# Performance work log

Hardware: AMD Instinct MI355X
Metric: run time of the kernel (lower is better)

## Reference

```python
import jax, jax.numpy as jnp
import numpy as np

N_TREES, DEPTH, INPUT_DIM, N_CLASSES = 15, 3, 128, 10
N_LEAVES = 2 ** DEPTH
N_INTERNAL = N_LEAVES - 1


def _path_masks(depth):
    """Right/left ancestor indicator matrices [n_leaves, n_internal]."""
    n_leaves = 2 ** depth
    n_int = n_leaves - 1
    R = np.zeros((n_leaves, n_int), np.float32)
    L = np.zeros((n_leaves, n_int), np.float32)
    for leaf in range(n_leaves):
        node = leaf + n_int
        for _ in range(depth):
            parent = (node - 1) // 2
            if node % 2 == 0:
                R[leaf, parent] = 1.0
            else:
                L[leaf, parent] = 1.0
            node = parent
    return R, L

_R, _L = _path_masks(DEPTH)


def setup_inputs() -> dict:
    key = jax.random.key(0)
    k1, k2 = jax.random.split(key)
    batch = 262144
    per_tree = N_INTERNAL * INPUT_DIM + N_INTERNAL + N_LEAVES * N_CLASSES
    total = N_TREES * per_tree + N_TREES
    x = jax.random.normal(k1, (batch, INPUT_DIM), dtype=jnp.float32)
    params = jax.random.normal(k2, (total,), dtype=jnp.float32)
    return {"x": x, "params": params}


def reference(x, params):
    per_tree = N_INTERNAL * INPUT_DIM + N_INTERNAL + N_LEAVES * N_CLASSES
    blocks = params[: N_TREES * per_tree].reshape(N_TREES, per_tree)
    w_end = N_INTERNAL * INPUT_DIM
    split_w = blocks[:, :w_end].reshape(N_TREES, N_INTERNAL, INPUT_DIM)
    split_b = blocks[:, w_end : w_end + N_INTERNAL]  # [T, n_internal]
    leaf_logits = blocks[:, w_end + N_INTERNAL :].reshape(N_TREES, N_LEAVES, N_CLASSES)
    tree_w_logits = params[N_TREES * per_tree :]  # [T]

    # split logits z: [B, T, n_internal]
    z = jnp.einsum("bd,tnd->btn", x, split_w) + split_b[None, :, :]
    log_p = jax.nn.log_sigmoid(z)        # log sigma(z)
    log_1mp = jax.nn.log_sigmoid(-z)     # log (1 - sigma(z))

    R = jnp.asarray(_R)
    L = jnp.asarray(_L)
    # path product in log domain: [B, T, n_leaves]
    leaf_probs = jnp.exp(
        jnp.einsum("btn,ln->btl", log_p, R) + jnp.einsum("btn,ln->btl", log_1mp, L)
    )

    leaf_class_probs = jax.nn.softmax(leaf_logits, axis=-1)  # [T, n_leaves, C]
    tree_pred = jnp.einsum("btl,tlc->btc", leaf_probs, leaf_class_probs)
    tree_weights = jax.nn.softmax(tree_w_logits, axis=0)     # [T]
    final_pred = jnp.einsum("btc,t->bc", tree_pred, tree_weights)
    return final_pred
```

## Files before the change

### kernel.cpp

```cpp
#include <hip/hip_runtime.h>
#include <hip/hip_fp16.h>


typedef float    f32x4 __attribute__((ext_vector_type(4)));
typedef _Float16 half8 __attribute__((ext_vector_type(8)));

#define TREES      15
#define IDIM       128
#define NCLS       10
#define NINT       7
#define NLVS       8
#define PER_TREE   (NINT*IDIM + NINT + NLVS*NCLS)
#define NODES      (TREES*NINT)
#define NPAD       112
#define KPAD       128
#define RSTR       272
#define WSTR       4352
#define NBLK       512

__global__ __launch_bounds__(256) void prep_kernel(const float* __restrict__ p,
                                                   _Float16* __restrict__ wq,
                                                   float* __restrict__ bq,
                                                   _Float16* __restrict__ wbT) {
    const int gid  = blockIdx.x * 256 + threadIdx.x;
    const int nthr = gridDim.x * 256;

    for (int i = gid; i < NPAD * IDIM; i += nthr) {
        int g = i >> 7, k = i & 127;
        float v = 0.f;
        if (g < NODES) {
            int t = g / NINT, n = g % NINT;
            v = p[t * PER_TREE + n * IDIM + k];
        }
        wq[i] = (_Float16)v;
    }
    for (int i = gid; i < NPAD; i += nthr) {
        float v = 0.f;
        if (i < NODES) {
            int t = i / NINT, n = i % NINT;
            v = p[t * PER_TREE + NINT * IDIM + n];
        }
        bq[i] = v;
    }
    const float* tl = p + TREES * PER_TREE;
    for (int i = gid; i < 16 * KPAD; i += nthr) {
        int c = i >> 7, k = i & 127;
        float v = 0.f;
        if (c < NCLS && k < TREES * NLVS) {
            int t = k >> 3, l = k & 7;
            const float* ll = p + t * PER_TREE + NINT * IDIM + NINT + l * NCLS;
            float mx = ll[0];
            #pragma unroll
            for (int j = 1; j < NCLS; ++j) mx = fmaxf(mx, ll[j]);
            float se = 0.f;
            #pragma unroll
            for (int j = 0; j < NCLS; ++j) se += __expf(ll[j] - mx);
            float lsm = __expf(ll[c] - mx) / se;

            float m2 = tl[0];
            #pragma unroll
            for (int j = 1; j < TREES; ++j) m2 = fmaxf(m2, tl[j]);
            float s2 = 0.f;
            #pragma unroll
            for (int j = 0; j < TREES; ++j) s2 += __expf(tl[j] - m2);
            float tw = __expf(tl[t] - m2) / s2;
            v = lsm * tw;
        }
        wbT[i] = (_Float16)v;
    }
}

__device__ __forceinline__ void load_xa(const float* __restrict__ xr,
                                        f32x4 (&xa)[8]) {
    #pragma unroll
    for (int s = 0; s < 4; ++s) {
        xa[2 * s]     = *(const f32x4*)(xr + 32 * s);
        xa[2 * s + 1] = *(const f32x4*)(xr + 32 * s + 4);
    }
}

__global__ __launch_bounds__(256, 2) void tree_main(const float* __restrict__ x,
                                                    const _Float16* __restrict__ wq,
                                                    const float* __restrict__ bq,
                                                    const _Float16* __restrict__ wbT,
                                                    float* __restrict__ out,
                                                    int tpb) {
    __shared__ __align__(16) char lds[4 * WSTR];

    const int tid  = threadIdx.x;
    const int lane = tid & 63;
    const int w    = tid >> 6;
    const int lm   = lane & 15;
    const int lq   = lane >> 4;
    const int rg   = lane >> 2;
    const int g    = lane & 3;

    char* sbuf = &lds[w * WSTR];
    const long tile0 = (long)blockIdx.x * tpb;

    const float* xlane = x + (tile0 * 64 + 16 * w + lm) * IDIM + 8 * lq;

    f32x4 xaA[8], xaB[8];
    load_xa(xlane, xaA);

    half8 bf[7][4];
    float bb[7];
    #pragma unroll
    for (int nt = 0; nt < 7; ++nt) {
        bb[nt] = bq[16 * nt + lm];
        #pragma unroll
        for (int s = 0; s < 4; ++s)
            bf[nt][s] = *reinterpret_cast<const half8*>(wq + (16 * nt + lm) * IDIM + 32 * s + 8 * lq);
    }
    half8 wbf[4];
    #pragma unroll
    for (int s = 0; s < 4; ++s)
        wbf[s] = *reinterpret_cast<const half8*>(wbT + lm * KPAD + 32 * s + 8 * lq);

    auto tile_body = [&](int i, f32x4 (&xac)[8], f32x4 (&xan)[8]) {
        const long grow = (tile0 + i) * 64;

        half8 af[4];
        #pragma unroll
        for (int s = 0; s < 4; ++s) {
            half8 a;
            #pragma unroll
            for (int j = 0; j < 4; ++j) {
                a[j]     = (_Float16)xac[2 * s][j];
                a[j + 4] = (_Float16)xac[2 * s + 1][j];
            }
            af[s] = a;
        }

        if (i + 1 < tpb)
            load_xa(xlane + (long)(i + 1) * 64 * IDIM, xan);

        #pragma unroll
        for (int nt = 0; nt < 7; ++nt) {
            f32x4 acc = {bb[nt], bb[nt], bb[nt], bb[nt]};
            #pragma unroll
            for (int s = 0; s < 4; ++s)
                acc = __builtin_amdgcn_mfma_f32_16x16x32_f16(af[s], bf[nt][s], acc, 0, 0, 0);
            int node = 16 * nt + lm;
            int col  = node + ((node * 9363) >> 16);
            #pragma unroll
            for (int r = 0; r < 4; ++r) {
                float z  = acc[r];
                float sg = __builtin_amdgcn_rcpf(1.0f + __expf(-z));
                *(_Float16*)(sbuf + (4 * lq + r) * RSTR + col * 2) = (_Float16)sg;
            }
        }

        {
            const char* rowp = sbuf + rg * RSTR;
            half8 hv[4];
            #pragma unroll
            for (int tt = 0; tt < 4; ++tt)
                hv[tt] = *(const half8*)(rowp + 64 * g + 16 * tt);
            half8 lv[4];
            #pragma unroll
            for (int tt = 0; tt < 4; ++tt) {
                float s0 = (float)hv[tt][0], s1 = (float)hv[tt][1], s2v = (float)hv[tt][2];
                float s3 = (float)hv[tt][3], s4 = (float)hv[tt][4], s5 = (float)hv[tt][5];
                float s6 = (float)hv[tt][6];
                float u1 = 1.f - s0, u2 = s0;
                float q1 = u1 * s1, q0 = u1 - q1;
                float q3 = u2 * s2v, q2 = u2 - q3;
                float L1 = q0 * s3, L0 = q0 - L1;
                float L3 = q1 * s4, L2 = q1 - L3;
                float L5 = q2 * s5, L4 = q2 - L5;
                float L7 = q3 * s6, L6 = q3 - L7;
                float m = (4 * g + tt < TREES) ? 1.f : 0.f;
                half8 lv8;
                lv8[0] = (_Float16)(L0 * m); lv8[1] = (_Float16)(L1 * m);
                lv8[2] = (_Float16)(L2 * m); lv8[3] = (_Float16)(L3 * m);
                lv8[4] = (_Float16)(L4 * m); lv8[5] = (_Float16)(L5 * m);
                lv8[6] = (_Float16)(L6 * m); lv8[7] = (_Float16)(L7 * m);
                lv[tt] = lv8;
            }
            #pragma unroll
            for (int tt = 0; tt < 4; ++tt)
                *(half8*)(sbuf + rg * RSTR + 64 * g + 16 * tt) = lv[tt];
        }

        {
            half8 af2[4];
            #pragma unroll
            for (int s = 0; s < 4; ++s)
                af2[s] = *(const half8*)(sbuf + lm * RSTR + 64 * s + 16 * lq);
            f32x4 a2 = {0.f, 0.f, 0.f, 0.f};
            #pragma unroll
            for (int s = 0; s < 4; ++s)
                a2 = __builtin_amdgcn_mfma_f32_16x16x32_f16(af2[s], wbf[s], a2, 0, 0, 0);
            if (lm < NCLS) {
                #pragma unroll
                for (int r = 0; r < 4; ++r)
                    out[(grow + 16 * w + 4 * lq + r) * NCLS + lm] = a2[r];
            }
        }
    };

    for (int i = 0; i < tpb; i += 2) {
        tile_body(i,     xaA, xaB);
        tile_body(i + 1, xaB, xaA);
    }
}

extern "C" void kernel_launch(void* const* d_in, const int* in_sizes, int n_in,
                              void* d_out, int out_size, void* d_ws, size_t ws_size,
                              hipStream_t stream) {
    const float* x      = (const float*)d_in[0];
    const float* params = (const float*)d_in[1];
    float* out = (float*)d_out;

    _Float16* wq  = (_Float16*)d_ws;
    float*    bq  = (float*)((char*)d_ws + NPAD * IDIM * 2);
    _Float16* wbT = (_Float16*)((char*)bq + NPAD * 4);

    const int batch = in_sizes[0] / IDIM;
    const int tiles = batch / 64;
    const int tpb   = tiles / NBLK;

    prep_kernel<<<8, 256, 0, stream>>>(params, wq, bq, wbT);
    tree_main<<<NBLK, 256, 0, stream>>>(x, wq, bq, wbT, out, tpb);
}
```

Measured before the change: 208.4 us.

## Stage split weights in swizzled LDS and double block size for occupancy

```diff
diff --git a/kernel.cpp b/kernel.cpp
--- a/kernel.cpp
+++ b/kernel.cpp
@@ -79,13 +79,14 @@
     }
 }
 
-__global__ __launch_bounds__(256, 2) void tree_main(const float* __restrict__ x,
+__global__ __launch_bounds__(512, 4) void tree_main(const float* __restrict__ x,
                                                     const _Float16* __restrict__ wq,
                                                     const float* __restrict__ bq,
                                                     const _Float16* __restrict__ wbT,
                                                     float* __restrict__ out,
                                                     int tpb) {
-    __shared__ __align__(16) char lds[4 * WSTR];
+    __shared__ __align__(16) char lwq[NPAD * 256];
+    __shared__ __align__(16) char sls[8 * WSTR];
 
     const int tid  = threadIdx.x;
     const int lane = tid & 63;
@@ -95,30 +96,37 @@
     const int rg   = lane >> 2;
     const int g    = lane & 3;
 
-    char* sbuf = &lds[w * WSTR];
+    char* sbuf = &sls[w * WSTR];
     const long tile0 = (long)blockIdx.x * tpb;
 
-    const float* xlane = x + (tile0 * 64 + 16 * w + lm) * IDIM + 8 * lq;
-
-    f32x4 xaA[8], xaB[8];
-    load_xa(xlane, xaA);
-
-    half8 bf[7][4];
+    const float* xlane = x + (tile0 * 128 + 16 * w + lm) * IDIM + 8 * lq;
+
+    f32x4 xa[8];
+    load_xa(xlane, xa);
+
+    for (int k = tid; k < NPAD * 16; k += 512) {
+        int row = k >> 4, c = k & 15;
+        half8 v = *reinterpret_cast<const half8*>(wq + row * 128 + c * 8);
+        *(half8*)(lwq + row * 256 + (((c + row) & 15) << 4)) = v;
+    }
+
     float bb[7];
     #pragma unroll
-    for (int nt = 0; nt < 7; ++nt) {
-        bb[nt] = bq[16 * nt + lm];
-        #pragma unroll
-        for (int s = 0; s < 4; ++s)
-            bf[nt][s] = *reinterpret_cast<const half8*>(wq + (16 * nt + lm) * IDIM + 32 * s + 8 * lq);
-    }
+    for (int nt = 0; nt < 7; ++nt) bb[nt] = bq[16 * nt + lm];
     half8 wbf[4];
     #pragma unroll
     for (int s = 0; s < 4; ++s)
         wbf[s] = *reinterpret_cast<const half8*>(wbT + lm * KPAD + 32 * s + 8 * lq);
 
-    auto tile_body = [&](int i, f32x4 (&xac)[8], f32x4 (&xan)[8]) {
-        const long grow = (tile0 + i) * 64;
+    int addr_s[4];
+    #pragma unroll
+    for (int s = 0; s < 4; ++s)
+        addr_s[s] = lm * 256 + (((4 * s + lq + lm) & 15) << 4);
+
+    __syncthreads();
+
+    for (int i = 0; i < tpb; ++i) {
+        const long grow = (tile0 + i) * 128;
 
         half8 af[4];
         #pragma unroll
@@ -126,21 +134,20 @@
             half8 a;
             #pragma unroll
             for (int j = 0; j < 4; ++j) {
-                a[j]     = (_Float16)xac[2 * s][j];
-                a[j + 4] = (_Float16)xac[2 * s + 1][j];
+                a[j]     = (_Float16)xa[2 * s][j];
+                a[j + 4] = (_Float16)xa[2 * s + 1][j];
             }
             af[s] = a;
         }
 
         if (i + 1 < tpb)
-            load_xa(xlane + (long)(i + 1) * 64 * IDIM, xan);
-
-        #pragma unroll
-        for (int nt = 0; nt < 7; ++nt) {
+            load_xa(xlane + (long)(i + 1) * 128 * IDIM, xa);
+
+        auto pa_compute = [&](int nt, half8 (&bf)[4]) {
             f32x4 acc = {bb[nt], bb[nt], bb[nt], bb[nt]};
             #pragma unroll
             for (int s = 0; s < 4; ++s)
-                acc = __builtin_amdgcn_mfma_f32_16x16x32_f16(af[s], bf[nt][s], acc, 0, 0, 0);
+                acc = __builtin_amdgcn_mfma_f32_16x16x32_f16(af[s], bf[s], acc, 0, 0, 0);
             int node = 16 * nt + lm;
             int col  = node + ((node * 9363) >> 16);
             #pragma unroll
@@ -149,7 +156,24 @@
                 float sg = __builtin_amdgcn_rcpf(1.0f + __expf(-z));
                 *(_Float16*)(sbuf + (4 * lq + r) * RSTR + col * 2) = (_Float16)sg;
             }
-        }
+        };
+        half8 bfA[4], bfB[4];
+        #pragma unroll
+        for (int s = 0; s < 4; ++s)
+            bfA[s] = *(const half8*)(lwq + addr_s[s]);
+        #pragma unroll 1
+        for (int ntp = 0; ntp < 3; ++ntp) {
+            const int base = ntp * 8192;
+            #pragma unroll
+            for (int s = 0; s < 4; ++s)
+                bfB[s] = *(const half8*)(lwq + addr_s[s] + base + 4096);
+            pa_compute(2 * ntp, bfA);
+            #pragma unroll
+            for (int s = 0; s < 4; ++s)
+                bfA[s] = *(const half8*)(lwq + addr_s[s] + base + 8192);
+            pa_compute(2 * ntp + 1, bfB);
+        }
+        pa_compute(6, bfA);
 
         {
             const char* rowp = sbuf + rg * RSTR;
@@ -198,11 +222,6 @@
                     out[(grow + 16 * w + 4 * lq + r) * NCLS + lm] = a2[r];
             }
         }
-    };
-
-    for (int i = 0; i < tpb; i += 2) {
-        tile_body(i,     xaA, xaB);
-        tile_body(i + 1, xaB, xaA);
     }
 }
 
@@ -218,9 +237,9 @@
     _Float16* wbT = (_Float16*)((char*)bq + NPAD * 4);
 
     const int batch = in_sizes[0] / IDIM;
-    const int tiles = batch / 64;
+    const int tiles = batch / 128;
     const int tpb   = tiles / NBLK;
 
     prep_kernel<<<8, 256, 0, stream>>>(params, wq, bq, wbT);
-    tree_main<<<NBLK, 256, 0, stream>>>(x, wq, bq, wbT, out, tpb);
-}
+    tree_main<<<NBLK, 512, 0, stream>>>(x, wq, bq, wbT, out, tpb);
+}
```

Result: slower. 214.4 us (+2.9%).
